# Kernel tuning notes

Measured on AMD Instinct MI355X. Metric: run time of the kernel, lower is better.

## Reference

```python
import jax, jax.numpy as jnp
import numpy as np

EPS_REG = 0.1  # entropic regularization (forward arg eps_regularization in the torch module)


def _cosine_dist(a, b):
    # pairwise cosine distance: 1 - <a_i/|a_i|, b_j/|b_j|>
    an = a / jnp.linalg.norm(a, axis=-1, keepdims=True)
    bn = b / jnp.linalg.norm(b, axis=-1, keepdims=True)
    return 1.0 - an @ bn.T  # [n, m]


def _sinkhorn(C, eps, n_iters):
    # log-domain Sinkhorn with uniform marginals on a stack of k cost matrices [k, n, m]
    k, n, m = C.shape
    loga = -jnp.log(jnp.asarray(n, C.dtype))
    logb = -jnp.log(jnp.asarray(m, C.dtype))
    f0 = jnp.zeros((k, n), C.dtype)
    g0 = jnp.zeros((k, m), C.dtype)

    def step(carry, _):
        f, g = carry
        M = (-C + f[:, :, None] + g[:, None, :]) / eps
        f = f + eps * (loga - jax.nn.logsumexp(M, axis=2))
        M = (-C + f[:, :, None] + g[:, None, :]) / eps
        g = g + eps * (logb - jax.nn.logsumexp(M, axis=1))
        return (f, g), None

    (f, g), _ = jax.lax.scan(step, (f0, g0), None, length=n_iters)
    # transport plans
    return jnp.exp((-C + f[:, :, None] + g[:, None, :]) / eps)


def setup_inputs() -> dict:
    key = jax.random.key(0)
    ks = jax.random.split(key, 6)
    B, D_in, D_e = 1024, 3072, 256
    mk = lambda k: jax.random.normal(k, (B, D_in), jnp.float32)
    return {
        "x": mk(ks[0]),
        "x_prime": mk(ks[1]),
        "y": mk(ks[2]),
        "y_prime": mk(ks[3]),
        "Wc": jax.random.normal(ks[4], (D_in, D_e), jnp.float32) / np.sqrt(D_in),
        "bc": jnp.zeros((D_e,), jnp.float32),
        "nb_sinkhorn_iterations": 20,
    }


def reference(x, x_prime, y, y_prime, Wc, bc, nb_sinkhorn_iterations):
    critic = lambda t: t @ Wc + bc  # stand-in for the external Critic network
    fx, fxp = critic(x), critic(x_prime)
    fy, fyp = critic(y), critic(y_prime)
    # C_11, C_12, C_21, C_22, C_rr, C_ff stacked: [6, B, B]
    C = jnp.stack([
        _cosine_dist(fx, fy),
        _cosine_dist(fx, fyp),
        _cosine_dist(fxp, fy),
        _cosine_dist(fxp, fyp),
        _cosine_dist(fx, fxp),
        _cosine_dist(fy, fyp),
    ])
    P = _sinkhorn(C, EPS_REG, nb_sinkhorn_iterations)  # [6, B, B]
    W = jnp.sum(P * C, axis=(1, 2))  # W_11, W_12, W_21, W_22, W_rr, W_ff
    signs = jnp.array([1.0, 1.0, 1.0, 1.0, -2.0, -2.0], C.dtype)
    return jnp.sum(signs * W)
```

## Files before the change

### kernel.cpp

```cpp
#include <hip/hip_runtime.h>
#include <hip/hip_fp16.h>
#include <math.h>

#define BN 1024
#define DIN 3072
#define DE 256
#define NK 6
#define KS 8
#define GBLKH 768
#define RPBH 8
#define GBLKW 384
#define RPBW 16
#define MAXIT 20
#define BM 64
#define BNC 128
#define KSTEP 32
#define LDA 40

constexpr float K2F = 14.4269504088896340736f;

typedef short short8 __attribute__((ext_vector_type(8)));
typedef float float4v __attribute__((ext_vector_type(4)));
typedef unsigned short ushort4v __attribute__((ext_vector_type(4)));

__device__ __forceinline__ unsigned short f2bf(float x) {
  union { float f; unsigned u; } v; v.f = x;
  unsigned r = v.u + 0x7FFF + ((v.u >> 16) & 1);
  return (unsigned short)(r >> 16);
}
__device__ __forceinline__ float bf2f(unsigned short h) {
  union { float f; unsigned u; } v; v.u = ((unsigned)h) << 16;
  return v.f;
}

__global__ __launch_bounds__(256) void wct_prep(
    const float* __restrict__ Wc, unsigned short* __restrict__ WcTh,
    unsigned short* __restrict__ WcTl) {
  __shared__ float tile[64][65];
  const int t = threadIdx.x;
  const int kb = blockIdx.x * 64, cb = blockIdx.y * 64;
#pragma unroll
  for (int i = 0; i < 4; ++i) {
    int k = (t >> 4) + i * 16;
    int c = (t & 15) * 4;
    float4 v = *(const float4*)&Wc[(size_t)(kb + k) * DE + cb + c];
    tile[k][c] = v.x; tile[k][c + 1] = v.y; tile[k][c + 2] = v.z; tile[k][c + 3] = v.w;
  }
  __syncthreads();
#pragma unroll
  for (int i = 0; i < 4; ++i) {
    int c = (t >> 4) + i * 16;
    int k = (t & 15) * 4;
    ushort4v h, l;
#pragma unroll
    for (int j = 0; j < 4; ++j) {
      float v = tile[k + j][c];
      unsigned short hh = f2bf(v);
      h[j] = hh; l[j] = f2bf(v - bf2f(hh));
    }
    *(ushort4v*)&WcTh[(size_t)(cb + c) * DIN + kb + k] = h;
    *(ushort4v*)&WcTl[(size_t)(cb + c) * DIN + kb + k] = l;
  }
}

__global__ __launch_bounds__(256) void critic_mfma(
    const float* __restrict__ x, const float* __restrict__ xp,
    const float* __restrict__ y, const float* __restrict__ yp,
    const unsigned short* __restrict__ WcTh,
    const unsigned short* __restrict__ WcTl, float* __restrict__ Pp) {
  __shared__ unsigned short Ah[BM][LDA], Al[BM][LDA];
  __shared__ unsigned short Bh[BNC][LDA], Bl[BNC][LDA];
  const int t = threadIdx.x;
  const int rt = blockIdx.x, ct = blockIdx.y, ks = blockIdx.z;
  const int R0 = rt * BM;
  const int m = R0 >> 10, r0 = R0 & 1023;
  const float* src = (m == 0) ? x : (m == 1) ? xp : (m == 2) ? y : yp;
  const int wid = t >> 6, lane = t & 63;
  const int wy = wid >> 1, wx = wid & 1;
  const int fr = lane & 15, fg = lane >> 4;

  float4v acc[2][4];
#pragma unroll
  for (int i = 0; i < 2; ++i)
#pragma unroll
    for (int j = 0; j < 4; ++j) acc[i][j] = (float4v){0.f, 0.f, 0.f, 0.f};

  const int kbase = ks * (DIN / KS);
  for (int k0 = 0; k0 < DIN / KS; k0 += KSTEP) {
    const int kg = kbase + k0;
    __syncthreads();
    {
      int row = t >> 2, kq = (t & 3) * 8;
      const float* ap = src + (size_t)(r0 + row) * DIN + kg + kq;
      float4 a0 = *(const float4*)(ap);
      float4 a1 = *(const float4*)(ap + 4);
      float av[8] = {a0.x, a0.y, a0.z, a0.w, a1.x, a1.y, a1.z, a1.w};
      short8 h0, l0;
#pragma unroll
      for (int j = 0; j < 8; ++j) {
        unsigned short h = f2bf(av[j]);
        h0[j] = (short)h; l0[j] = (short)f2bf(av[j] - bf2f(h));
      }
      *(short8*)&Ah[row][kq] = h0;
      *(short8*)&Al[row][kq] = l0;
    }
    {
      int col = t >> 1, kq = (t & 1) * 16;
      const unsigned short* bph = WcTh + (size_t)(ct * BNC + col) * DIN + kg + kq;
      const unsigned short* bpl = WcTl + (size_t)(ct * BNC + col) * DIN + kg + kq;
      short8 h0 = *(const short8*)(bph);
      short8 h1 = *(const short8*)(bph + 8);
      short8 l0 = *(const short8*)(bpl);
      short8 l1 = *(const short8*)(bpl + 8);
      *(short8*)&Bh[col][kq] = h0; *(short8*)&Bh[col][kq + 8] = h1;
      *(short8*)&Bl[col][kq] = l0; *(short8*)&Bl[col][kq + 8] = l1;
    }
    __syncthreads();
    short8 afh[2], afl[2], bfh[4], bfl[4];
#pragma unroll
    for (int i = 0; i < 2; ++i) {
      int row = wy * 32 + i * 16 + fr;
      afh[i] = *(const short8*)&Ah[row][fg * 8];
      afl[i] = *(const short8*)&Al[row][fg * 8];
    }
#pragma unroll
    for (int j = 0; j < 4; ++j) {
      int col = wx * 64 + j * 16 + fr;
      bfh[j] = *(const short8*)&Bh[col][fg * 8];
      bfl[j] = *(const short8*)&Bl[col][fg * 8];
    }
#pragma unroll
    for (int i = 0; i < 2; ++i)
#pragma unroll
      for (int j = 0; j < 4; ++j) {
        acc[i][j] = __builtin_amdgcn_mfma_f32_16x16x32_bf16(afh[i], bfh[j], acc[i][j], 0, 0, 0);
        acc[i][j] = __builtin_amdgcn_mfma_f32_16x16x32_bf16(afh[i], bfl[j], acc[i][j], 0, 0, 0);
        acc[i][j] = __builtin_amdgcn_mfma_f32_16x16x32_bf16(afl[i], bfh[j], acc[i][j], 0, 0, 0);
      }
  }
#pragma unroll
  for (int i = 0; i < 2; ++i)
#pragma unroll
    for (int j = 0; j < 4; ++j) {
      int grow = R0 + wy * 32 + i * 16 + fg * 4;
      int gcol = ct * BNC + wx * 64 + j * 16 + fr;
#pragma unroll
      for (int reg = 0; reg < 4; ++reg)
        Pp[((size_t)ks * 4096 + grow + reg) * DE + gcol] = acc[i][j][reg];
    }
}

__global__ __launch_bounds__(256) void critic_norm(
    const float* __restrict__ Pp, const float* __restrict__ bc,
    unsigned short* __restrict__ Fh, unsigned short* __restrict__ Fl) {
  __shared__ double red[4];
  __shared__ double nrm2s;
  const int row = blockIdx.x, t = threadIdx.x;
  double val = (double)bc[t];
#pragma unroll
  for (int ks = 0; ks < KS; ++ks)
    val += (double)Pp[((size_t)ks * 4096 + row) * DE + t];
  double ss = val * val;
#pragma unroll
  for (int off = 32; off; off >>= 1) ss += __shfl_down(ss, off);
  if ((t & 63) == 0) red[t >> 6] = ss;
  __syncthreads();
  if (t == 0) nrm2s = red[0] + red[1] + red[2] + red[3];
  __syncthreads();
  float fv = (float)(val / sqrt(nrm2s));
  unsigned short h = f2bf(fv);
  Fh[(size_t)row * DE + t] = h;
  Fl[(size_t)row * DE + t] = f2bf(fv - bf2f(h));
}

__global__ __launch_bounds__(256) void cosine_mfma(
    const unsigned short* __restrict__ Fh, const unsigned short* __restrict__ Fl,
    __half* __restrict__ E, __half* __restrict__ ET) {
  __shared__ unsigned short Ah[128][LDA], Al[128][LDA];
  __shared__ unsigned short Bh[128][LDA], Bl[128][LDA];
  const int pa[NK] = {0, 0, 1, 1, 0, 2};
  const int pb[NK] = {2, 3, 2, 3, 1, 3};
  const int p = blockIdx.z;
  const int ti = blockIdx.y, tj = blockIdx.x;
  const int t = threadIdx.x;
  const int wid = t >> 6, lane = t & 63;
  const int wy = wid >> 1, wx = wid & 1;
  const int fr = lane & 15, fg = lane >> 4;
  const size_t rbase = (size_t)(pa[p] * BN + ti * 128) * DE;
  const size_t cbase = (size_t)(pb[p] * BN + tj * 128) * DE;

  float4v acc[4][4];
#pragma unroll
  for (int i = 0; i < 4; ++i)
#pragma unroll
    for (int j = 0; j < 4; ++j) acc[i][j] = (float4v){0.f, 0.f, 0.f, 0.f};

  for (int kg = 0; kg < DE; kg += KSTEP) {
    __syncthreads();
    {
      int row = t >> 1, kq = (t & 1) * 16;
      const unsigned short* ah = Fh + rbase + (size_t)row * DE + kg + kq;
      const unsigned short* al = Fl + rbase + (size_t)row * DE + kg + kq;
      *(short8*)&Ah[row][kq] = *(const short8*)(ah);
      *(short8*)&Ah[row][kq + 8] = *(const short8*)(ah + 8);
      *(short8*)&Al[row][kq] = *(const short8*)(al);
      *(short8*)&Al[row][kq + 8] = *(const short8*)(al + 8);
      const unsigned short* bh = Fh + cbase + (size_t)row * DE + kg + kq;
      const unsigned short* bl = Fl + cbase + (size_t)row * DE + kg + kq;
      *(short8*)&Bh[row][kq] = *(const short8*)(bh);
      *(short8*)&Bh[row][kq + 8] = *(const short8*)(bh + 8);
      *(short8*)&Bl[row][kq] = *(const short8*)(bl);
      *(short8*)&Bl[row][kq + 8] = *(const short8*)(bl + 8);
    }
    __syncthreads();
    short8 afh[4], afl[4], bfh[4], bfl[4];
#pragma unroll
    for (int i = 0; i < 4; ++i) {
      int row = wy * 64 + i * 16 + fr;
      afh[i] = *(const short8*)&Ah[row][fg * 8];
      afl[i] = *(const short8*)&Al[row][fg * 8];
      int col = wx * 64 + i * 16 + fr;
      bfh[i] = *(const short8*)&Bh[col][fg * 8];
      bfl[i] = *(const short8*)&Bl[col][fg * 8];
    }
#pragma unroll
    for (int i = 0; i < 4; ++i)
#pragma unroll
      for (int j = 0; j < 4; ++j) {
        acc[i][j] = __builtin_amdgcn_mfma_f32_16x16x32_bf16(afh[i], bfh[j], acc[i][j], 0, 0, 0);
        acc[i][j] = __builtin_amdgcn_mfma_f32_16x16x32_bf16(afh[i], bfl[j], acc[i][j], 0, 0, 0);
        acc[i][j] = __builtin_amdgcn_mfma_f32_16x16x32_bf16(afl[i], bfh[j], acc[i][j], 0, 0, 0);
      }
  }
#pragma unroll
  for (int i = 0; i < 4; ++i)
#pragma unroll
    for (int j = 0; j < 4; ++j) {
      int grow0 = ti * 128 + wy * 64 + i * 16 + fg * 4;
      int gcol = tj * 128 + wx * 64 + j * 16 + fr;
      union { __half h[4]; uint2 w; } pk;
#pragma unroll
      for (int reg = 0; reg < 4; ++reg)
        pk.h[reg] = __float2half(exp2f(acc[i][j][reg] * K2F));
      __half* ep = E + ((size_t)p << 20) + (size_t)grow0 * BN + gcol;
#pragma unroll
      for (int reg = 0; reg < 4; ++reg) ep[(size_t)reg * BN] = pk.h[reg];
      *reinterpret_cast<uint2*>(ET + ((size_t)p << 20) + ((size_t)gcol << 10) + grow0) = pk.w;
    }
}

__device__ __forceinline__ float fold4(float s0, float s1, float s2, float s3,
                                       int lane) {
  float a01 = ((lane & 32) ? s1 : s0) + __shfl_xor(((lane & 32) ? s0 : s1), 32);
  float a23 = ((lane & 32) ? s3 : s2) + __shfl_xor(((lane & 32) ? s2 : s3), 32);
  float z = ((lane & 16) ? a23 : a01) + __shfl_xor(((lane & 16) ? a01 : a23), 16);
#pragma unroll
  for (int off = 8; off; off >>= 1) z += __shfl_xor(z, off);
  return z;
}

template <int NR>
__device__ __forceinline__ void load_rowsN(const __half* M, int R0, int t,
                                           uint2 (&w)[NR]) {
  const uint2* Mb = reinterpret_cast<const uint2*>(M) + ((size_t)R0 << 8);
#pragma unroll
  for (int r = 0; r < NR; ++r) w[r] = Mb[(r << 8) + t];
}

template <int NR, bool WSUM>
__device__ __forceinline__ void phase_rowsN(const uint2 (&w)[NR], float4 uv,
                                            float* red, int t) {
  const int lane = t & 63, wv = t >> 6;
#pragma unroll
  for (int g = 0; g < NR / 4; ++g) {
    float s[4];
#pragma unroll
    for (int r = 0; r < 4; ++r) {
      uint2 ww = w[g * 4 + r];
      float2 f0 = __half22float2(*reinterpret_cast<const __half2*>(&ww.x));
      float2 f1 = __half22float2(*reinterpret_cast<const __half2*>(&ww.y));
      if (WSUM) {
        s[r] = f0.x * uv.x * (1.f - 0.1f * __logf(f0.x)) +
               f0.y * uv.y * (1.f - 0.1f * __logf(f0.y)) +
               f1.x * uv.z * (1.f - 0.1f * __logf(f1.x)) +
               f1.y * uv.w * (1.f - 0.1f * __logf(f1.y));
      } else {
        s[r] = f0.x * uv.x + f0.y * uv.y + f1.x * uv.z + f1.y * uv.w;
      }
    }
    float z = fold4(s[0], s[1], s[2], s[3], lane);
    if ((lane & 15) == 0) {
      int lg = lane >> 4;
      int row = ((lg & 1) << 1) | (lg >> 1);
      red[wv * NR + g * 4 + row] = z;
    }
  }
}

__global__ __launch_bounds__(256) void fb_init(float* __restrict__ u) {
  int i = blockIdx.x * 256 + threadIdx.x;
  if (i < 2 * NK * BN) u[i] = 1.f;
}

__global__ __launch_bounds__(256) void fb_half(
    const __half* __restrict__ M, const float* __restrict__ uin,
    float* __restrict__ uout, int it, const int* __restrict__ nit) {
  if (it >= *nit) return;
  __shared__ float red[4 * RPBH];
  const int t = threadIdx.x, b = blockIdx.x;
  const int R0 = b * RPBH, k = R0 >> 10;
  uint2 w[RPBH];
  load_rowsN<RPBH>(M, R0, t, w);
  phase_rowsN<RPBH, false>(w, reinterpret_cast<const float4*>(uin + (k << 10))[t], red, t);
  __syncthreads();
  if (t < RPBH) {
    float S = red[t] + red[RPBH + t] + red[2 * RPBH + t] + red[3 * RPBH + t];
    uout[R0 + t] = 1.f / (1024.f * S);
  }
}

__global__ __launch_bounds__(256) void fb_wsum(
    const __half* __restrict__ E, const float* __restrict__ uf,
    const float* __restrict__ ug, double* __restrict__ Wp) {
  __shared__ float red[4 * RPBW];
  __shared__ double red2[RPBW];
  const int t = threadIdx.x, b = blockIdx.x;
  const int R0 = b * RPBW, k = R0 >> 10;
  uint2 w[RPBW];
  load_rowsN<RPBW>(E, R0, t, w);
  phase_rowsN<RPBW, true>(w, reinterpret_cast<const float4*>(ug + (k << 10))[t], red, t);
  __syncthreads();
  if (t < RPBW)
    red2[t] = (double)(red[t] + red[RPBW + t] + red[2 * RPBW + t] + red[3 * RPBW + t]) *
              (double)uf[R0 + t];
  __syncthreads();
  if (t == 0) {
    double bp = 0.0;
#pragma unroll
    for (int r = 0; r < RPBW; ++r) bp += red2[r];
    Wp[b] = ((k < 4) ? 1.0 : -2.0) * bp;
  }
}

__global__ __launch_bounds__(256) void fb_final(
    const double* __restrict__ Wp, float* __restrict__ out) {
  __shared__ double redf[4];
  const int t = threadIdx.x;
  double p = 0.0;
  for (int i = t; i < GBLKW; i += 256) p += Wp[i];
#pragma unroll
  for (int off = 32; off; off >>= 1) p += __shfl_down(p, off);
  if ((t & 63) == 0) redf[t >> 6] = p;
  __syncthreads();
  if (t == 0) out[0] = (float)(redf[0] + redf[1] + redf[2] + redf[3]);
}

extern "C" void kernel_launch(void* const* d_in, const int* in_sizes, int n_in,
                              void* d_out, int out_size, void* d_ws, size_t ws_size,
                              hipStream_t stream) {
  (void)in_sizes; (void)n_in; (void)out_size; (void)ws_size;
  const float* x  = (const float*)d_in[0];
  const float* xp = (const float*)d_in[1];
  const float* y  = (const float*)d_in[2];
  const float* yp = (const float*)d_in[3];
  const float* Wc = (const float*)d_in[4];
  const float* bc = (const float*)d_in[5];
  const int*  nit = (const int*)d_in[6];

  char* ws = (char*)d_ws;
  const size_t MB = 1024 * 1024;
  const size_t szEh = (size_t)NK * BN * BN * 2;
  float*  Pp  = (float*)(ws);
  __half* Eh  = (__half*)(ws);
  __half* EhT = (__half*)(ws + szEh);
  unsigned short* Fh   = (unsigned short*)(ws + 34 * MB);
  unsigned short* Fl   = (unsigned short*)(ws + 37 * MB);
  unsigned short* WcTh = (unsigned short*)(ws + 40 * MB);
  unsigned short* WcTl = (unsigned short*)(ws + 42 * MB);
  float*  uf = (float*)(ws + 44 * MB);
  float*  ug = uf + NK * BN;
  double* Wp = (double*)(ug + NK * BN);

  wct_prep<<<dim3(DIN / 64, DE / 64), 256, 0, stream>>>(Wc, WcTh, WcTl);
  critic_mfma<<<dim3(4096 / BM, DE / BNC, KS), 256, 0, stream>>>(
      x, xp, y, yp, WcTh, WcTl, Pp);
  critic_norm<<<4096, 256, 0, stream>>>(Pp, bc, Fh, Fl);
  cosine_mfma<<<dim3(BN / 128, BN / 128, NK), 256, 0, stream>>>(Fh, Fl, Eh, EhT);

  fb_init<<<48, 256, 0, stream>>>(uf);
  for (int it = 0; it < MAXIT; ++it) {
    fb_half<<<GBLKH, 256, 0, stream>>>(Eh, ug, uf, it, nit);
    fb_half<<<GBLKH, 256, 0, stream>>>(EhT, uf, ug, it, nit);
  }
  fb_wsum<<<GBLKW, 256, 0, stream>>>(Eh, uf, ug, Wp);
  fb_final<<<1, 256, 0, stream>>>(Wp, (float*)d_out);
}
```

Before: 212.3 us.

## Enlarge critic GEMM row tile, halve rows per Sinkhorn block, drop init kernel

The critic GEMM block tile doubles from 64 to 128 rows, so each wave computes a 64x64 output with 4x4 MFMA accumulators and every B fragment is reused across more rows. The Sinkhorn half-step kernels now handle 4 rows per block with twice as many blocks, aiming at better occupancy and spread across CUs. The fb_init kernel is removed and the first half-step uses a templated path with a constant vector of ones, saving one launch. The cost is higher register pressure in the GEMM and half as many GEMM blocks, which may lower occupancy there.

```diff
diff --git a/kernel.cpp b/kernel.cpp
--- a/kernel.cpp
+++ b/kernel.cpp
@@ -7,12 +7,12 @@
 #define DE 256
 #define NK 6
 #define KS 8
-#define GBLKH 768
-#define RPBH 8
+#define GBLKH 1536
+#define RPBH 4
 #define GBLKW 384
 #define RPBW 16
 #define MAXIT 20
-#define BM 64
+#define BM 128
 #define BNC 128
 #define KSTEP 32
 #define LDA 40
@@ -79,9 +79,9 @@
   const int wy = wid >> 1, wx = wid & 1;
   const int fr = lane & 15, fg = lane >> 4;
 
-  float4v acc[2][4];
-#pragma unroll
-  for (int i = 0; i < 2; ++i)
+  float4v acc[4][4];
+#pragma unroll
+  for (int i = 0; i < 4; ++i)
 #pragma unroll
     for (int j = 0; j < 4; ++j) acc[i][j] = (float4v){0.f, 0.f, 0.f, 0.f};
 
@@ -90,19 +90,24 @@
     const int kg = kbase + k0;
     __syncthreads();
     {
-      int row = t >> 2, kq = (t & 3) * 8;
+      int row = t >> 1, kq = (t & 1) * 16;
       const float* ap = src + (size_t)(r0 + row) * DIN + kg + kq;
       float4 a0 = *(const float4*)(ap);
       float4 a1 = *(const float4*)(ap + 4);
-      float av[8] = {a0.x, a0.y, a0.z, a0.w, a1.x, a1.y, a1.z, a1.w};
-      short8 h0, l0;
+      float4 a2 = *(const float4*)(ap + 8);
+      float4 a3 = *(const float4*)(ap + 12);
+      float av[16] = {a0.x, a0.y, a0.z, a0.w, a1.x, a1.y, a1.z, a1.w,
+                      a2.x, a2.y, a2.z, a2.w, a3.x, a3.y, a3.z, a3.w};
+      short8 h0, h1, l0, l1;
 #pragma unroll
       for (int j = 0; j < 8; ++j) {
         unsigned short h = f2bf(av[j]);
         h0[j] = (short)h; l0[j] = (short)f2bf(av[j] - bf2f(h));
+        unsigned short g = f2bf(av[j + 8]);
+        h1[j] = (short)g; l1[j] = (short)f2bf(av[j + 8] - bf2f(g));
       }
-      *(short8*)&Ah[row][kq] = h0;
-      *(short8*)&Al[row][kq] = l0;
+      *(short8*)&Ah[row][kq] = h0; *(short8*)&Ah[row][kq + 8] = h1;
+      *(short8*)&Al[row][kq] = l0; *(short8*)&Al[row][kq + 8] = l1;
     }
     {
       int col = t >> 1, kq = (t & 1) * 16;
@@ -116,21 +121,18 @@
       *(short8*)&Bl[col][kq] = l0; *(short8*)&Bl[col][kq + 8] = l1;
     }
     __syncthreads();
-    short8 afh[2], afl[2], bfh[4], bfl[4];
-#pragma unroll
-    for (int i = 0; i < 2; ++i) {
-      int row = wy * 32 + i * 16 + fr;
+    short8 afh[4], afl[4], bfh[4], bfl[4];
+#pragma unroll
+    for (int i = 0; i < 4; ++i) {
+      int row = wy * 64 + i * 16 + fr;
       afh[i] = *(const short8*)&Ah[row][fg * 8];
       afl[i] = *(const short8*)&Al[row][fg * 8];
-    }
-#pragma unroll
-    for (int j = 0; j < 4; ++j) {
-      int col = wx * 64 + j * 16 + fr;
-      bfh[j] = *(const short8*)&Bh[col][fg * 8];
-      bfl[j] = *(const short8*)&Bl[col][fg * 8];
-    }
-#pragma unroll
-    for (int i = 0; i < 2; ++i)
+      int col = wx * 64 + i * 16 + fr;
+      bfh[i] = *(const short8*)&Bh[col][fg * 8];
+      bfl[i] = *(const short8*)&Bl[col][fg * 8];
+    }
+#pragma unroll
+    for (int i = 0; i < 4; ++i)
 #pragma unroll
       for (int j = 0; j < 4; ++j) {
         acc[i][j] = __builtin_amdgcn_mfma_f32_16x16x32_bf16(afh[i], bfh[j], acc[i][j], 0, 0, 0);
@@ -139,10 +141,10 @@
       }
   }
 #pragma unroll
-  for (int i = 0; i < 2; ++i)
+  for (int i = 0; i < 4; ++i)
 #pragma unroll
     for (int j = 0; j < 4; ++j) {
-      int grow = R0 + wy * 32 + i * 16 + fg * 4;
+      int grow = R0 + wy * 64 + i * 16 + fg * 4;
       int gcol = ct * BNC + wx * 64 + j * 16 + fr;
 #pragma unroll
       for (int reg = 0; reg < 4; ++reg)
@@ -297,11 +299,7 @@
   }
 }
 
-__global__ __launch_bounds__(256) void fb_init(float* __restrict__ u) {
-  int i = blockIdx.x * 256 + threadIdx.x;
-  if (i < 2 * NK * BN) u[i] = 1.f;
-}
-
+template <bool FIRST>
 __global__ __launch_bounds__(256) void fb_half(
     const __half* __restrict__ M, const float* __restrict__ uin,
     float* __restrict__ uout, int it, const int* __restrict__ nit) {
@@ -311,7 +309,10 @@
   const int R0 = b * RPBH, k = R0 >> 10;
   uint2 w[RPBH];
   load_rowsN<RPBH>(M, R0, t, w);
-  phase_rowsN<RPBH, false>(w, reinterpret_cast<const float4*>(uin + (k << 10))[t], red, t);
+  float4 uv;
+  if (FIRST) uv = make_float4(1.f, 1.f, 1.f, 1.f);
+  else uv = reinterpret_cast<const float4*>(uin + (k << 10))[t];
+  phase_rowsN<RPBH, false>(w, uv, red, t);
   __syncthreads();
   if (t < RPBH) {
     float S = red[t] + red[RPBH + t] + red[2 * RPBH + t] + red[3 * RPBH + t];
@@ -387,10 +388,11 @@
   critic_norm<<<4096, 256, 0, stream>>>(Pp, bc, Fh, Fl);
   cosine_mfma<<<dim3(BN / 128, BN / 128, NK), 256, 0, stream>>>(Fh, Fl, Eh, EhT);
 
-  fb_init<<<48, 256, 0, stream>>>(uf);
-  for (int it = 0; it < MAXIT; ++it) {
-    fb_half<<<GBLKH, 256, 0, stream>>>(Eh, ug, uf, it, nit);
-    fb_half<<<GBLKH, 256, 0, stream>>>(EhT, uf, ug, it, nit);
+  fb_half<true><<<GBLKH, 256, 0, stream>>>(Eh, nullptr, uf, 0, nit);
+  fb_half<false><<<GBLKH, 256, 0, stream>>>(EhT, uf, ug, 0, nit);
+  for (int it = 1; it < MAXIT; ++it) {
+    fb_half<false><<<GBLKH, 256, 0, stream>>>(Eh, ug, uf, it, nit);
+    fb_half<false><<<GBLKH, 256, 0, stream>>>(EhT, uf, ug, it, nit);
   }
   fb_wsum<<<GBLKW, 256, 0, stream>>>(Eh, uf, ug, Wp);
   fb_final<<<1, 256, 0, stream>>>(Wp, (float*)d_out);
```

Result: faster. 206.8 us (median of 2 runs) (-2.6%).
